# Performance work log

Hardware: AMD Instinct MI355X
Metric: run time of the kernel (lower is better)

Reference implementation:

```python
import jax, jax.numpy as jnp
import numpy as np

N = 100000
E = 3200000
B = 8192
IN_DIM = 18   # enc_dim for khops=2
HID = 64
EMB = 32


def setup_inputs() -> dict:
    key = jax.random.key(0)
    ks = jax.random.split(key, 10)
    x = jax.random.normal(ks[0], (N, IN_DIM), dtype=jnp.float32)
    ei = jax.random.randint(ks[1], (2, E), 0, N, dtype=jnp.int64)
    targets = jax.random.randint(ks[2], (2, B), 0, N, dtype=jnp.int64)
    # GCN layer params (glorot-ish scale)
    W1 = jax.random.normal(ks[3], (IN_DIM, HID), dtype=jnp.float32) / np.sqrt(IN_DIM)
    b1 = jnp.zeros((HID,), dtype=jnp.float32)
    W2 = jax.random.normal(ks[4], (HID, EMB), dtype=jnp.float32) / np.sqrt(HID)
    b2 = jnp.zeros((EMB,), dtype=jnp.float32)
    Wo = jax.random.normal(ks[5], (EMB, 1), dtype=jnp.float32) / np.sqrt(EMB)
    bo = jnp.zeros((1,), dtype=jnp.float32)
    return {"x": x, "ei": ei, "targets": targets,
            "W1": W1, "b1": b1, "W2": W2, "b2": b2, "Wo": Wo, "bo": bo}


def _gcn_conv(x, W, b, src, dst, norm, n_nodes):
    # x' = D^{-1/2}(A+I)D^{-1/2} X W + b  (self-loops already in src/dst)
    h = x @ W                                  # [N, F_out]
    msg = h[src] * norm[:, None]               # [E+N, F_out] gather
    agg = jax.ops.segment_sum(msg, dst, num_segments=n_nodes)  # scatter-add
    return agg + b


def reference(x, ei, targets, W1, b1, W2, b2, Wo, bo):
    n = x.shape[0]
    loop = jnp.arange(n, dtype=ei.dtype)
    src = jnp.concatenate([ei[0], loop])
    dst = jnp.concatenate([ei[1], loop])
    deg = jax.ops.segment_sum(jnp.ones_like(src, dtype=x.dtype), dst, num_segments=n)
    dis = jax.lax.rsqrt(deg)                   # deg >= 1 (self-loops)
    norm = dis[src] * dis[dst]
    # 2-layer GCN (khops=2): relu between layers, dropout=0 (eval)
    h = jax.nn.relu(_gcn_conv(x, W1, b1, src, dst, norm, n))
    z = _gcn_conv(h, W2, b2, src, dst, norm, n)
    # node-pair multiply + linear head
    pair = z[targets[0]] * z[targets[1]]       # [B, EMB]
    return pair @ Wo + bo                      # [B, 1]
```

## Files before the change

### kernel.cpp

```cpp
#include <hip/hip_runtime.h>

#define IN_DIM 18
#define XPAD 20
#define HID 64
#define EMB 32
#define NGROUP 8
#define PSHIFT 9
#define PMAX 200
#define BCAP 80
#define TILE 8192
#define SCAP 16896

typedef int vint4 __attribute__((ext_vector_type(4)));
typedef unsigned long long u64;

__device__ inline float4 shfl_f4(float4 v, int srcLane) {
    float4 r;
    r.x = __shfl(v.x, srcLane);
    r.y = __shfl(v.y, srcLane);
    r.z = __shfl(v.z, srcLane);
    r.w = __shfl(v.w, srcLane);
    return r;
}

__device__ inline float4 shfl_xor_f4(float4 v, int m) {
    v.x = __shfl_xor(v.x, m);
    v.y = __shfl_xor(v.y, m);
    v.z = __shfl_xor(v.z, m);
    v.w = __shfl_xor(v.w, m);
    return v;
}


__global__ void k_init(int* __restrict__ deg, int* __restrict__ gcnt, int n) {
    int i = blockIdx.x * 256 + threadIdx.x;
    if (i < n) deg[i] = 1;
    if (i < 256) gcnt[i] = 0;
}


__global__ void k_part(const int* __restrict__ src, const int* __restrict__ dst,
                       int* __restrict__ gcnt, u64* __restrict__ gbuf,
                       int e, int Pp, int cap) {
    __shared__ u64 sbuf[PMAX][BCAP];
    __shared__ int scnt[PMAX];
    __shared__ int sbase[PMAX];
    int tid = threadIdx.x;
    int ntile = (e + TILE - 1) / TILE;
    for (int tile = blockIdx.x; tile < ntile; tile += gridDim.x) {
        for (int p = tid; p < Pp; p += 256) scnt[p] = 0;
        __syncthreads();
#pragma unroll
        for (int r = 0; r < TILE / 1024; ++r) {
            int i = tile * TILE + (r * 256 + tid) * 4;
            if (i + 4 <= e) {
                vint4 s4 = __builtin_nontemporal_load((const vint4*)(src + i));
                vint4 d4 = __builtin_nontemporal_load((const vint4*)(dst + i));
#pragma unroll
                for (int k = 0; k < 4; ++k) {
                    int d = d4[k];
                    int p = d >> PSHIFT;
                    u64 pr = ((u64)(unsigned)s4[k] << 32) | (unsigned)d;
                    int pos = atomicAdd(&scnt[p], 1);
                    if (pos < BCAP) sbuf[p][pos] = pr;
                    else {
                        int gp = atomicAdd(&gcnt[p], 1);
                        __builtin_nontemporal_store(pr, &gbuf[(size_t)p * cap + gp]);
                    }
                }
            } else if (i < e) {
                for (int k = i; k < e; ++k) {
                    int d = dst[k];
                    int p = d >> PSHIFT;
                    u64 pr = ((u64)(unsigned)src[k] << 32) | (unsigned)d;
                    int pos = atomicAdd(&scnt[p], 1);
                    if (pos < BCAP) sbuf[p][pos] = pr;
                    else {
                        int gp = atomicAdd(&gcnt[p], 1);
                        __builtin_nontemporal_store(pr, &gbuf[(size_t)p * cap + gp]);
                    }
                }
            }
        }
        __syncthreads();
        for (int p = tid; p < Pp; p += 256)
            sbase[p] = atomicAdd(&gcnt[p], min(scnt[p], BCAP));
        __syncthreads();
        int wid = tid >> 6, lane = tid & 63;
        for (int p = wid; p < Pp; p += 4) {
            int c = min(scnt[p], BCAP);
            int b = sbase[p];
            for (int k = lane; k < c; k += 64)
                __builtin_nontemporal_store(sbuf[p][k], &gbuf[(size_t)p * cap + b + k]);
        }
        __syncthreads();
    }
}


__global__ void k_gscan(const int* __restrict__ gcnt, int* __restrict__ gbase, int Pp) {
    __shared__ int s[256];
    int t = threadIdx.x;
    int v = (t < Pp) ? gcnt[t] : 0;
    s[t] = v;
    __syncthreads();
    for (int off = 1; off < 256; off <<= 1) {
        int u = (t >= off) ? s[t - off] : 0;
        __syncthreads();
        s[t] += u;
        __syncthreads();
    }
    if (t < Pp) gbase[t] = s[t] - v;
}


__global__ void k_build(const u64* __restrict__ gbuf, const int* __restrict__ gcnt,
                        const int* __restrict__ gbase, int* __restrict__ deg,
                        float* __restrict__ dis, int* __restrict__ row_ptr,
                        int* __restrict__ adj, int cap, int n) {
    __shared__ u64 spairs[SCAP];
    __shared__ int sdeg[512];
    __shared__ int sexcl[512];
    __shared__ int swp[512];
    __shared__ int sscan[256];
    int p = blockIdx.x;
    int tid = threadIdx.x;
    int lo = p << PSHIFT;
    int nn = min(n - lo, 512);
    int cnt = gcnt[p];
    int base = gbase[p];
    const u64* buf = gbuf + (size_t)p * cap;

    sdeg[tid] = 0; sdeg[tid + 256] = 0;
    int scap = min(cnt, SCAP);
    for (int k = tid; k < scap; k += 256)
        spairs[k] = __builtin_nontemporal_load(&buf[k]);
    __syncthreads();
    for (int k = tid; k < cnt; k += 256) {
        u64 pr = (k < SCAP) ? spairs[k] : __builtin_nontemporal_load(&buf[k]);
        atomicAdd(&sdeg[(int)(pr & 0xffffffffu) - lo], 1);
    }
    __syncthreads();
    int e0 = sdeg[2 * tid], e1 = sdeg[2 * tid + 1];
    sscan[tid] = e0 + e1;
    __syncthreads();
    for (int off = 1; off < 256; off <<= 1) {
        int u = (tid >= off) ? sscan[tid - off] : 0;
        __syncthreads();
        sscan[tid] += u;
        __syncthreads();
    }
    int before = (tid > 0) ? sscan[tid - 1] : 0;
    sexcl[2 * tid] = before;
    sexcl[2 * tid + 1] = before + e0;
    swp[tid] = 0; swp[tid + 256] = 0;
    __syncthreads();
    for (int i = tid; i < nn; i += 256) {
        int dg = sdeg[i] + 1;
        deg[lo + i] = dg;
        dis[lo + i] = rsqrtf((float)dg);
        row_ptr[lo + i] = base + sexcl[i];
    }
    for (int k = tid; k < cnt; k += 256) {
        u64 pr = (k < SCAP) ? spairs[k] : __builtin_nontemporal_load(&buf[k]);
        int dl = (int)(pr & 0xffffffffu) - lo;
        int slot = sexcl[dl] + atomicAdd(&swp[dl], 1);
        adj[base + slot] = (int)(pr >> 32);
    }
}


__global__ void k_count_part(const int* __restrict__ dst, int* __restrict__ deg,
                             int e, int nrange, int n) {
    int g  = blockIdx.x & (NGROUP - 1);
    int lo = g * nrange;
    int hi = min(n, lo + nrange);
    int bid  = blockIdx.x >> 3;
    int nblk = gridDim.x >> 3;
    int i0   = (bid * 256 + threadIdx.x) * 4;
    int step = nblk * 256 * 4;
    for (int i = i0; i < e; i += step) {
        if (i + 4 <= e) {
            int4 d4 = *(const int4*)(dst + i);
            if (d4.x >= lo && d4.x < hi) atomicAdd(&deg[d4.x], 1);
            if (d4.y >= lo && d4.y < hi) atomicAdd(&deg[d4.y], 1);
            if (d4.z >= lo && d4.z < hi) atomicAdd(&deg[d4.z], 1);
            if (d4.w >= lo && d4.w < hi) atomicAdd(&deg[d4.w], 1);
        } else {
            for (int k = i; k < e; ++k) {
                int d = dst[k];
                if (d >= lo && d < hi) atomicAdd(&deg[d], 1);
            }
        }
    }
}

__global__ void k_dis(const int* __restrict__ deg, float* __restrict__ dis, int n) {
    int i = blockIdx.x * 256 + threadIdx.x;
    if (i < n) dis[i] = rsqrtf((float)deg[i]);
}

__global__ void k_scanA(const int* __restrict__ deg, int* __restrict__ row_ptr,
                        int* __restrict__ blksums, int n) {
    __shared__ int s[1024];
    int tid = threadIdx.x;
    int i = blockIdx.x * 1024 + tid;
    int v = (i < n) ? (deg[i] - 1) : 0;
    s[tid] = v;
    __syncthreads();
    for (int off = 1; off < 1024; off <<= 1) {
        int t = (tid >= off) ? s[tid - off] : 0;
        __syncthreads();
        s[tid] += t;
        __syncthreads();
    }
    if (i < n) row_ptr[i] = s[tid] - v;
    if (tid == 1023) blksums[blockIdx.x] = s[1023];
}

__global__ void k_scanB(const int* __restrict__ blksums, int* __restrict__ blkoffs, int nb) {
    __shared__ int s[1024];
    int tid = threadIdx.x;
    int v = (tid < nb) ? blksums[tid] : 0;
    s[tid] = v;
    __syncthreads();
    for (int off = 1; off < 1024; off <<= 1) {
        int t = (tid >= off) ? s[tid - off] : 0;
        __syncthreads();
        s[tid] += t;
        __syncthreads();
    }
    if (tid < nb) blkoffs[tid] = s[tid] - v;
}

__global__ void k_scanC(int* __restrict__ row_ptr, const int* __restrict__ blkoffs,
                        int* __restrict__ write_ptr, int n) {
    int i = blockIdx.x * 1024 + threadIdx.x;
    if (i < n) {
        int r = row_ptr[i] + blkoffs[blockIdx.x];
        row_ptr[i] = r;
        write_ptr[i] = r;
    }
}

__global__ void k_fill_part(const int* __restrict__ src, const int* __restrict__ dst,
                            int* __restrict__ write_ptr, int* __restrict__ adj,
                            int e, int nrange, int n) {
    int g  = blockIdx.x & (NGROUP - 1);
    int lo = g * nrange;
    int hi = min(n, lo + nrange);
    int bid  = blockIdx.x >> 3;
    int nblk = gridDim.x >> 3;
    int i0   = (bid * 256 + threadIdx.x) * 4;
    int step = nblk * 256 * 4;
    for (int i = i0; i < e; i += step) {
        if (i + 4 <= e) {
            int4 d4 = *(const int4*)(dst + i);
            if (d4.x >= lo && d4.x < hi) { int slot = atomicAdd(&write_ptr[d4.x], 1); adj[slot] = src[i];     }
            if (d4.y >= lo && d4.y < hi) { int slot = atomicAdd(&write_ptr[d4.y], 1); adj[slot] = src[i + 1]; }
            if (d4.z >= lo && d4.z < hi) { int slot = atomicAdd(&write_ptr[d4.z], 1); adj[slot] = src[i + 2]; }
            if (d4.w >= lo && d4.w < hi) { int slot = atomicAdd(&write_ptr[d4.w], 1); adj[slot] = src[i + 3]; }
        } else {
            for (int k = i; k < e; ++k) {
                int d = dst[k];
                if (d >= lo && d < hi) { int slot = atomicAdd(&write_ptr[d], 1); adj[slot] = src[k]; }
            }
        }
    }
}


__global__ void k_xn(const float* __restrict__ x, const float* __restrict__ dis,
                     float* __restrict__ xn, int n) {
    int gid = blockIdx.x * 256 + threadIdx.x;
    if (gid >= n * 5) return;
    int i = gid / 5, s = gid - (gid / 5) * 5;
    float dn = dis[i];
    const float* xr = x + (size_t)i * IN_DIM;
    float4 v;
    int k = s * 4;
    v.x = (k + 0 < IN_DIM) ? xr[k + 0] * dn : 0.f;
    v.y = (k + 1 < IN_DIM) ? xr[k + 1] * dn : 0.f;
    v.z = (k + 2 < IN_DIM) ? xr[k + 2] * dn : 0.f;
    v.w = (k + 3 < IN_DIM) ? xr[k + 3] * dn : 0.f;
    *(float4*)(xn + (size_t)i * XPAD + k) = v;
}


__global__ void k_agg1f(const float* __restrict__ xn, const int* __restrict__ row_ptr,
                        const int* __restrict__ deg, const int* __restrict__ adj,
                        const float* __restrict__ dis, const float* __restrict__ W1,
                        const float* __restrict__ b1, float* __restrict__ h, int n) {
    __shared__ float sw[IN_DIM * HID];
    __shared__ float sb[HID];
    __shared__ __align__(16) float sagg[4][XPAD];
    int tid = threadIdx.x;
    for (int t = tid; t < IN_DIM * HID; t += 256) sw[t] = W1[t];
    if (tid < HID) sb[tid] = b1[tid];
    __syncthreads();
    int node = blockIdx.x * 4 + (tid >> 6);
    if (node >= n) return;
    int lane = tid & 63;
    int wv = tid >> 6;
    int eg = lane / 5;
    int sl = lane - eg * 5;
    bool act = eg < 12;
    int beg = row_ptr[node];
    int cnt = deg[node] - 1;
    const int* a = adj + beg;
    float4 acc = make_float4(0.f, 0.f, 0.f, 0.f);
    int base = 0;
    for (; base + 24 <= cnt; base += 24) {
        if (act) {
            int j0 = a[base + eg];
            int j1 = a[base + 12 + eg];
            float4 v0 = *(const float4*)(xn + (size_t)j0 * XPAD + sl * 4);
            float4 v1 = *(const float4*)(xn + (size_t)j1 * XPAD + sl * 4);
            acc.x += v0.x + v1.x; acc.y += v0.y + v1.y;
            acc.z += v0.z + v1.z; acc.w += v0.w + v1.w;
        }
    }
    if (act && base + eg < cnt) {
        float4 v = *(const float4*)(xn + (size_t)a[base + eg] * XPAD + sl * 4);
        acc.x += v.x; acc.y += v.y; acc.z += v.z; acc.w += v.w;
    }
    if (act && base + 12 + eg < cnt) {
        float4 v = *(const float4*)(xn + (size_t)a[base + 12 + eg] * XPAD + sl * 4);
        acc.x += v.x; acc.y += v.y; acc.z += v.z; acc.w += v.w;
    }
    float4 t = shfl_f4(acc, lane + 30);
    if (lane < 30) { acc.x += t.x; acc.y += t.y; acc.z += t.z; acc.w += t.w; }
    t = shfl_f4(acc, lane + 15);
    if (lane < 15) { acc.x += t.x; acc.y += t.y; acc.z += t.z; acc.w += t.w; }
    t = shfl_f4(acc, lane + 10);
    if (lane < 5) { acc.x += t.x; acc.y += t.y; acc.z += t.z; acc.w += t.w; }
    t = shfl_f4(acc, lane + 5);
    if (lane < 5) { acc.x += t.x; acc.y += t.y; acc.z += t.z; acc.w += t.w; }
    if (lane < 5) {
        float4 s4v = *(const float4*)(xn + (size_t)node * XPAD + lane * 4);
        acc.x += s4v.x; acc.y += s4v.y; acc.z += s4v.z; acc.w += s4v.w;
        *(float4*)&sagg[wv][lane * 4] = acc;
    }
    float s = 0.f;
#pragma unroll
    for (int k = 0; k < IN_DIM; ++k) s += sagg[wv][k] * sw[k * HID + lane];
    float hv = dis[node] * s + sb[lane];
    h[(size_t)node * HID + lane] = hv > 0.f ? hv : 0.f;
}


__global__ void k_gemm2(const float* __restrict__ h, const float* __restrict__ W2,
                        const float* __restrict__ dis, float* __restrict__ hn2, int n) {
    __shared__ float w[HID * EMB];
    for (int t = threadIdx.x; t < HID * EMB; t += 256) w[t] = W2[t];
    __syncthreads();
    int gid = blockIdx.x * 256 + threadIdx.x;
    int i = gid >> 5, g = gid & 31;
    if (i >= n) return;
    const float* hr = h + (size_t)i * HID;
    float acc = 0.f;
#pragma unroll
    for (int k = 0; k < HID; ++k) acc += hr[k] * w[k * EMB + g];
    hn2[(size_t)i * EMB + g] = acc * dis[i];
}


__global__ void k_agg2(const float* __restrict__ hn2, const int* __restrict__ row_ptr,
                       const int* __restrict__ deg, const int* __restrict__ adj,
                       const float* __restrict__ dis, const float* __restrict__ b2,
                       float* __restrict__ z, int n) {
    int node = blockIdx.x * 4 + (threadIdx.x >> 6);
    if (node >= n) return;
    int lane = threadIdx.x & 63;
    int eg = lane >> 3;
    int d4 = lane & 7;
    int beg = row_ptr[node];
    int cnt = deg[node] - 1;
    const int* a = adj + beg;
    float4 acc = make_float4(0.f, 0.f, 0.f, 0.f);
    int base = 0;
    for (; base + 16 <= cnt; base += 16) {
        int j0 = a[base + eg];
        int j1 = a[base + 8 + eg];
        float4 v0 = *(const float4*)(hn2 + (size_t)j0 * EMB + d4 * 4);
        float4 v1 = *(const float4*)(hn2 + (size_t)j1 * EMB + d4 * 4);
        acc.x += v0.x + v1.x; acc.y += v0.y + v1.y;
        acc.z += v0.z + v1.z; acc.w += v0.w + v1.w;
    }
    int kk = base + eg;
    if (kk < cnt) {
        float4 v = *(const float4*)(hn2 + (size_t)a[kk] * EMB + d4 * 4);
        acc.x += v.x; acc.y += v.y; acc.z += v.z; acc.w += v.w;
    }
    kk += 8;
    if (kk < cnt) {
        float4 v = *(const float4*)(hn2 + (size_t)a[kk] * EMB + d4 * 4);
        acc.x += v.x; acc.y += v.y; acc.z += v.z; acc.w += v.w;
    }
    float4 t = shfl_xor_f4(acc, 8);
    acc.x += t.x; acc.y += t.y; acc.z += t.z; acc.w += t.w;
    t = shfl_xor_f4(acc, 16);
    acc.x += t.x; acc.y += t.y; acc.z += t.z; acc.w += t.w;
    t = shfl_xor_f4(acc, 32);
    acc.x += t.x; acc.y += t.y; acc.z += t.z; acc.w += t.w;
    if (eg == 0) {
        float4 self = *(const float4*)(hn2 + (size_t)node * EMB + d4 * 4);
        float4 bb = *(const float4*)(b2 + d4 * 4);
        float dn = dis[node];
        float4 o;
        o.x = dn * (acc.x + self.x) + bb.x;
        o.y = dn * (acc.y + self.y) + bb.y;
        o.z = dn * (acc.z + self.z) + bb.z;
        o.w = dn * (acc.w + self.w) + bb.w;
        *(float4*)(z + (size_t)node * EMB + d4 * 4) = o;
    }
}


__global__ void k_head(const float* __restrict__ z, const int* __restrict__ tg,
                       const float* __restrict__ Wo, const float* __restrict__ bo,
                       float* __restrict__ out, int btot) {
    int i = blockIdx.x * 256 + threadIdx.x;
    if (i >= btot) return;
    int t0 = tg[i], t1 = tg[btot + i];
    const float* z0 = z + (size_t)t0 * EMB;
    const float* z1 = z + (size_t)t1 * EMB;
    float acc = 0.f;
#pragma unroll
    for (int g = 0; g < EMB; ++g) acc += z0[g] * z1[g] * Wo[g];
    out[i] = acc + bo[0];
}


extern "C" void kernel_launch(void* const* d_in, const int* in_sizes, int n_in,
                              void* d_out, int out_size, void* d_ws, size_t ws_size,
                              hipStream_t stream) {
    const float* x  = (const float*)d_in[0];
    const int*   ei = (const int*)d_in[1];
    const int*   tg = (const int*)d_in[2];
    const float* W1 = (const float*)d_in[3];
    const float* b1 = (const float*)d_in[4];
    const float* W2 = (const float*)d_in[5];
    const float* b2 = (const float*)d_in[6];
    const float* Wo = (const float*)d_in[7];
    const float* bo = (const float*)d_in[8];
    float* out = (float*)d_out;

    int n = in_sizes[0] / IN_DIM;
    int e = in_sizes[1] / 2;
    int b = in_sizes[2] / 2;
    const int* src = ei;
    const int* dst = ei + e;

    char* ws = (char*)d_ws;
    size_t off = 0;
    auto alloc = [&](size_t bytes) -> char* {
        char* p = ws + off;
        off += (bytes + 255) & ~(size_t)255;
        return p;
    };
    int*   deg       = (int*)alloc((size_t)n * 4);
    int*   row_ptr   = (int*)alloc((size_t)n * 4);
    int*   write_ptr = (int*)alloc((size_t)n * 4);
    int*   blksums   = (int*)alloc(1024 * 4);
    int*   blkoffs   = (int*)alloc(1024 * 4);
    float* dis       = (float*)alloc((size_t)n * 4);
    int*   adj       = (int*)alloc((size_t)e * 4);
    float* xn        = (float*)alloc((size_t)n * XPAD * 4);
    float* bufA      = (float*)alloc((size_t)n * EMB * 4);
    float* bufB      = (float*)alloc((size_t)n * HID * 4);
    int*   gcnt      = (int*)alloc(1024);
    int*   gbase     = (int*)alloc(1024);

    int Pp = (n + 511) >> PSHIFT;
    int meanb = (Pp > 0) ? (e / Pp) : e;
    int cap = meanb + meanb / 16 + 1024;
    size_t bucket_bytes = (size_t)Pp * cap * 8;
    bool use_buckets = (Pp <= PMAX) && ((off + bucket_bytes + 256) <= ws_size);
    u64* gbuf = (u64*)alloc(bucket_bytes);

    int nb1024 = (n + 1023) / 1024;
    int nrange = (n + NGROUP - 1) / NGROUP;

    k_init<<<(n + 255) / 256, 256, 0, stream>>>(deg, gcnt, n);

    if (use_buckets) {
        k_part<<<256, 256, 0, stream>>>(src, dst, gcnt, gbuf, e, Pp, cap);
        k_gscan<<<1, 256, 0, stream>>>(gcnt, gbase, Pp);
        k_build<<<Pp, 256, 0, stream>>>(gbuf, gcnt, gbase, deg, dis, row_ptr, adj, cap, n);
    } else {
        k_count_part<<<2048, 256, 0, stream>>>(dst, deg, e, nrange, n);
        k_dis<<<(n + 255) / 256, 256, 0, stream>>>(deg, dis, n);
        k_scanA<<<nb1024, 1024, 0, stream>>>(deg, row_ptr, blksums, n);
        k_scanB<<<1, 1024, 0, stream>>>(blksums, blkoffs, nb1024);
        k_scanC<<<nb1024, 1024, 0, stream>>>(row_ptr, blkoffs, write_ptr, n);
        k_fill_part<<<2048, 256, 0, stream>>>(src, dst, write_ptr, adj, e, nrange, n);
    }

    k_xn<<<((size_t)n * 5 + 255) / 256, 256, 0, stream>>>(x, dis, xn, n);
    k_agg1f<<<(n + 3) / 4, 256, 0, stream>>>(xn, row_ptr, deg, adj, dis, W1, b1, bufB, n);
    k_gemm2<<<((size_t)n * EMB + 255) / 256, 256, 0, stream>>>(bufB, W2, dis, bufA, n);
    k_agg2<<<(n + 3) / 4, 256, 0, stream>>>(bufA, row_ptr, deg, adj, dis, b2, bufB, n);

    k_head<<<(b + 255) / 256, 256, 0, stream>>>(bufB, tg, Wo, bo, out, b);
}
```

Before: 270.3 us.

## Fuse second GEMM into layer-1 aggregation and retune build/partition kernels

Folds the HID-to-EMB projection into the first aggregation kernel through shared memory, so the N×64 hidden activations are never written to or re-read from global memory, and one kernel launch is dropped. The CSR build kernel now runs with 512 threads, one node per thread, using a 512-wide scan. The partition kernel gets twice the blocks with halved BCAP/TILE. The second aggregation is unrolled to three edge groups per iteration. The extra shared-memory W2 load per block and a sync-free read of sh written by other lanes in the same wavefront are the costs and risks.

```diff
diff --git a/kernel.cpp b/kernel.cpp
--- a/kernel.cpp
+++ b/kernel.cpp
@@ -7,8 +7,8 @@
 #define NGROUP 8
 #define PSHIFT 9
 #define PMAX 200
-#define BCAP 80
-#define TILE 8192
+#define BCAP 40
+#define TILE 4096
 #define SCAP 16896
 
 typedef int vint4 __attribute__((ext_vector_type(4)));
@@ -122,7 +122,7 @@
     __shared__ int sdeg[512];
     __shared__ int sexcl[512];
     __shared__ int swp[512];
-    __shared__ int sscan[256];
+    __shared__ int sscan[512];
     int p = blockIdx.x;
     int tid = threadIdx.x;
     int lo = p << PSHIFT;
@@ -131,37 +131,35 @@
     int base = gbase[p];
     const u64* buf = gbuf + (size_t)p * cap;
 
-    sdeg[tid] = 0; sdeg[tid + 256] = 0;
+    sdeg[tid] = 0;
     int scap = min(cnt, SCAP);
-    for (int k = tid; k < scap; k += 256)
+    for (int k = tid; k < scap; k += 512)
         spairs[k] = __builtin_nontemporal_load(&buf[k]);
     __syncthreads();
-    for (int k = tid; k < cnt; k += 256) {
+    for (int k = tid; k < cnt; k += 512) {
         u64 pr = (k < SCAP) ? spairs[k] : __builtin_nontemporal_load(&buf[k]);
         atomicAdd(&sdeg[(int)(pr & 0xffffffffu) - lo], 1);
     }
     __syncthreads();
-    int e0 = sdeg[2 * tid], e1 = sdeg[2 * tid + 1];
-    sscan[tid] = e0 + e1;
-    __syncthreads();
-    for (int off = 1; off < 256; off <<= 1) {
+    int v = sdeg[tid];
+    sscan[tid] = v;
+    __syncthreads();
+    for (int off = 1; off < 512; off <<= 1) {
         int u = (tid >= off) ? sscan[tid - off] : 0;
         __syncthreads();
         sscan[tid] += u;
         __syncthreads();
     }
-    int before = (tid > 0) ? sscan[tid - 1] : 0;
-    sexcl[2 * tid] = before;
-    sexcl[2 * tid + 1] = before + e0;
-    swp[tid] = 0; swp[tid + 256] = 0;
-    __syncthreads();
-    for (int i = tid; i < nn; i += 256) {
-        int dg = sdeg[i] + 1;
-        deg[lo + i] = dg;
-        dis[lo + i] = rsqrtf((float)dg);
-        row_ptr[lo + i] = base + sexcl[i];
-    }
-    for (int k = tid; k < cnt; k += 256) {
+    sexcl[tid] = sscan[tid] - v;
+    swp[tid] = 0;
+    __syncthreads();
+    if (tid < nn) {
+        int dg = sdeg[tid] + 1;
+        deg[lo + tid] = dg;
+        dis[lo + tid] = rsqrtf((float)dg);
+        row_ptr[lo + tid] = base + sexcl[tid];
+    }
+    for (int k = tid; k < cnt; k += 512) {
         u64 pr = (k < SCAP) ? spairs[k] : __builtin_nontemporal_load(&buf[k]);
         int dl = (int)(pr & 0xffffffffu) - lo;
         int slot = sexcl[dl] + atomicAdd(&swp[dl], 1);
@@ -290,12 +288,16 @@
 __global__ void k_agg1f(const float* __restrict__ xn, const int* __restrict__ row_ptr,
                         const int* __restrict__ deg, const int* __restrict__ adj,
                         const float* __restrict__ dis, const float* __restrict__ W1,
-                        const float* __restrict__ b1, float* __restrict__ h, int n) {
+                        const float* __restrict__ b1, const float* __restrict__ W2,
+                        float* __restrict__ hn2, int n) {
     __shared__ float sw[IN_DIM * HID];
+    __shared__ float sw2[HID * EMB];
     __shared__ float sb[HID];
     __shared__ __align__(16) float sagg[4][XPAD];
+    __shared__ float sh[4][HID];
     int tid = threadIdx.x;
     for (int t = tid; t < IN_DIM * HID; t += 256) sw[t] = W1[t];
+    for (int t = tid; t < HID * EMB; t += 256) sw2[t] = W2[t];
     if (tid < HID) sb[tid] = b1[tid];
     __syncthreads();
     int node = blockIdx.x * 4 + (tid >> 6);
@@ -336,6 +338,7 @@
     if (lane < 5) { acc.x += t.x; acc.y += t.y; acc.z += t.z; acc.w += t.w; }
     t = shfl_f4(acc, lane + 5);
     if (lane < 5) { acc.x += t.x; acc.y += t.y; acc.z += t.z; acc.w += t.w; }
+    float dn = dis[node];
     if (lane < 5) {
         float4 s4v = *(const float4*)(xn + (size_t)node * XPAD + lane * 4);
         acc.x += s4v.x; acc.y += s4v.y; acc.z += s4v.z; acc.w += s4v.w;
@@ -344,24 +347,14 @@
     float s = 0.f;
 #pragma unroll
     for (int k = 0; k < IN_DIM; ++k) s += sagg[wv][k] * sw[k * HID + lane];
-    float hv = dis[node] * s + sb[lane];
-    h[(size_t)node * HID + lane] = hv > 0.f ? hv : 0.f;
-}
-
-
-__global__ void k_gemm2(const float* __restrict__ h, const float* __restrict__ W2,
-                        const float* __restrict__ dis, float* __restrict__ hn2, int n) {
-    __shared__ float w[HID * EMB];
-    for (int t = threadIdx.x; t < HID * EMB; t += 256) w[t] = W2[t];
-    __syncthreads();
-    int gid = blockIdx.x * 256 + threadIdx.x;
-    int i = gid >> 5, g = gid & 31;
-    if (i >= n) return;
-    const float* hr = h + (size_t)i * HID;
-    float acc = 0.f;
+    float hv = dn * s + sb[lane];
+    sh[wv][lane] = hv > 0.f ? hv : 0.f;
+    int g = lane & 31, half = lane >> 5;
+    float s2 = 0.f;
 #pragma unroll
-    for (int k = 0; k < HID; ++k) acc += hr[k] * w[k * EMB + g];
-    hn2[(size_t)i * EMB + g] = acc * dis[i];
+    for (int k = 0; k < 32; ++k) s2 += sh[wv][half * 32 + k] * sw2[(half * 32 + k) * EMB + g];
+    s2 += __shfl_xor(s2, 32);
+    if (half == 0) hn2[(size_t)node * EMB + g] = dn * s2;
 }
 
 
@@ -379,15 +372,22 @@
     const int* a = adj + beg;
     float4 acc = make_float4(0.f, 0.f, 0.f, 0.f);
     int base = 0;
-    for (; base + 16 <= cnt; base += 16) {
+    for (; base + 24 <= cnt; base += 24) {
         int j0 = a[base + eg];
         int j1 = a[base + 8 + eg];
+        int j2 = a[base + 16 + eg];
         float4 v0 = *(const float4*)(hn2 + (size_t)j0 * EMB + d4 * 4);
         float4 v1 = *(const float4*)(hn2 + (size_t)j1 * EMB + d4 * 4);
-        acc.x += v0.x + v1.x; acc.y += v0.y + v1.y;
-        acc.z += v0.z + v1.z; acc.w += v0.w + v1.w;
+        float4 v2 = *(const float4*)(hn2 + (size_t)j2 * EMB + d4 * 4);
+        acc.x += v0.x + v1.x + v2.x; acc.y += v0.y + v1.y + v2.y;
+        acc.z += v0.z + v1.z + v2.z; acc.w += v0.w + v1.w + v2.w;
     }
     int kk = base + eg;
+    if (kk < cnt) {
+        float4 v = *(const float4*)(hn2 + (size_t)a[kk] * EMB + d4 * 4);
+        acc.x += v.x; acc.y += v.y; acc.z += v.z; acc.w += v.w;
+    }
+    kk += 8;
     if (kk < cnt) {
         float4 v = *(const float4*)(hn2 + (size_t)a[kk] * EMB + d4 * 4);
         acc.x += v.x; acc.y += v.y; acc.z += v.z; acc.w += v.w;
@@ -468,7 +468,7 @@
     int*   adj       = (int*)alloc((size_t)e * 4);
     float* xn        = (float*)alloc((size_t)n * XPAD * 4);
     float* bufA      = (float*)alloc((size_t)n * EMB * 4);
-    float* bufB      = (float*)alloc((size_t)n * HID * 4);
+    float* bufB      = (float*)alloc((size_t)n * EMB * 4);
     int*   gcnt      = (int*)alloc(1024);
     int*   gbase     = (int*)alloc(1024);
 
@@ -485,9 +485,9 @@
     k_init<<<(n + 255) / 256, 256, 0, stream>>>(deg, gcnt, n);
 
     if (use_buckets) {
-        k_part<<<256, 256, 0, stream>>>(src, dst, gcnt, gbuf, e, Pp, cap);
+        k_part<<<512, 256, 0, stream>>>(src, dst, gcnt, gbuf, e, Pp, cap);
         k_gscan<<<1, 256, 0, stream>>>(gcnt, gbase, Pp);
-        k_build<<<Pp, 256, 0, stream>>>(gbuf, gcnt, gbase, deg, dis, row_ptr, adj, cap, n);
+        k_build<<<Pp, 512, 0, stream>>>(gbuf, gcnt, gbase, deg, dis, row_ptr, adj, cap, n);
     } else {
         k_count_part<<<2048, 256, 0, stream>>>(dst, deg, e, nrange, n);
         k_dis<<<(n + 255) / 256, 256, 0, stream>>>(deg, dis, n);
@@ -498,8 +498,7 @@
     }
 
     k_xn<<<((size_t)n * 5 + 255) / 256, 256, 0, stream>>>(x, dis, xn, n);
-    k_agg1f<<<(n + 3) / 4, 256, 0, stream>>>(xn, row_ptr, deg, adj, dis, W1, b1, bufB, n);
-    k_gemm2<<<((size_t)n * EMB + 255) / 256, 256, 0, stream>>>(bufB, W2, dis, bufA, n);
+    k_agg1f<<<(n + 3) / 4, 256, 0, stream>>>(xn, row_ptr, deg, adj, dis, W1, b1, W2, bufA, n);
     k_agg2<<<(n + 3) / 4, 256, 0, stream>>>(bufA, row_ptr, deg, adj, dis, b2, bufB, n);
 
     k_head<<<(b + 255) / 256, 256, 0, stream>>>(bufB, tg, Wo, bo, out, b);
```

Result: faster. 239.2 us (-11.5%).
